# Kernel tuning notes

Hardware: AMD Instinct MI355X
Metric: run time of the kernel (lower is better)

Reference implementation:

```python
import jax, jax.numpy as jnp
import numpy as np

EMBED_DIM = 1024
SHIFT = 0.0

def setup_inputs() -> dict:
    key = jax.random.key(0)
    k1, k2, k3 = jax.random.split(key, 3)
    inputs = jax.random.normal(k1, (4, 2048, EMBED_DIM), dtype=jnp.float32)
    rotation_params = jax.random.normal(k2, (EMBED_DIM, EMBED_DIM), dtype=jnp.float32)
    entangle_params = jax.random.normal(k3, (EMBED_DIM, EMBED_DIM), dtype=jnp.float32)
    return {"inputs": inputs, "rotation_params": rotation_params, "entangle_params": entangle_params}

def reference(inputs, rotation_params, entangle_params):
    # inputs: (b, s, d)
    d = inputs.shape[-1]
    query = jnp.einsum('bsd,de->bse', inputs, rotation_params)
    key = jnp.einsum('bsd,de->bse', inputs, entangle_params)
    scores = jax.nn.softmax(jnp.einsum('bqd,bkd->bqk', query, key) / np.sqrt(d), axis=-1)
    out = jnp.einsum('bqk,bkd->bqd', scores, inputs)
    return jax.nn.sigmoid(out + SHIFT)
```

## Files before the change

kernel.cpp:

```cpp
#include <hip/hip_runtime.h>
#include <hip/hip_bf16.h>
#include <math.h>


using u16 = unsigned short;
using short8 = __attribute__((ext_vector_type(8))) short;
using f32x4  = __attribute__((ext_vector_type(4))) float;

#define MFB(a, b, c) __builtin_amdgcn_mfma_f32_16x16x32_bf16((a), (b), (c), 0, 0, 0)

__device__ static inline u16 f2bf(float f) {
    union { __hip_bfloat16 h; u16 u; } cv; cv.h = __float2bfloat16(f); return cv.u;
}
__device__ static inline float bf2f(u16 u) {
    union { __hip_bfloat16 h; u16 u; } cv; cv.u = u; return __bfloat162float(cv.h);
}
__device__ static inline void split2(float v, u16& h, u16& l) {
    h = f2bf(v);
    l = f2bf(v - bf2f(h));
}

__device__ static inline void gload16(const u16* g, u16* l) {
    __builtin_amdgcn_global_load_lds(
        (const __attribute__((address_space(1))) void*)g,
        (__attribute__((address_space(3))) void*)l, 16, 0, 0);
}

__device__ static inline short8 ldfrag(const u16* sm, int row, int g) {
    const int off = row * 32 + ((g ^ ((row >> 1) & 3)) << 3);
    return *reinterpret_cast<const short8*>(sm + off);
}

enum { EP_F32 = 0, EP_HILO = 1, EP_SIG = 2 };

template<int EPI, bool TRIPLE>
__global__ __launch_bounds__(256)
void gemm_split(const u16* __restrict__ Ahi, const u16* __restrict__ Alo,
                const u16* __restrict__ Bhi, const u16* __restrict__ Blo,
                float* __restrict__ Cf, u16* __restrict__ Chi, u16* __restrict__ Clo,
                int K, int lda, int ldb, int ldc,
                long sA, long sB, long sC, float alpha)
{
    const int z = blockIdx.z;
    Ahi += z * sA;
    Bhi += z * sB;
    if (TRIPLE) { Alo += z * sA; Blo += z * sB; }
    if (EPI == EP_HILO) { Chi += z * sC; Clo += z * sC; }
    else                { Cf  += z * sC; }

    constexpr int BUFSZ  = TRIPLE ? 16384 : 8192;
    constexpr int OFF_BH = TRIPLE ? 8192 : 4096;
    __shared__ __align__(16) u16 smem[2 * BUFSZ];

    const int t = threadIdx.x;
    const int wave = t >> 6, lane = t & 63;
    const int row0 = blockIdx.y * 128, col0 = blockIdx.x * 128;

    const int rr = t >> 2, cc = t & 3;
    const int gg = cc ^ ((rr >> 1) & 3);
    const u16* gAh = Ahi + (long)(row0 + rr) * lda + gg * 8;
    const u16* gBh = Bhi + (long)(col0 + rr) * ldb + gg * 8;
    const u16* gAl = TRIPLE ? (Alo + (long)(row0 + rr) * lda + gg * 8) : nullptr;
    const u16* gBl = TRIPLE ? (Blo + (long)(col0 + rr) * ldb + gg * 8) : nullptr;
    const long a2 = (long)64 * lda, b2 = (long)64 * ldb;

    f32x4 acc[4][4];
    #pragma unroll
    for (int m = 0; m < 4; m++)
        #pragma unroll
        for (int n = 0; n < 4; n++)
            acc[m][n] = (f32x4){0.f, 0.f, 0.f, 0.f};

    const int lr = lane & 15, lg = lane >> 4;
    const int wm = (wave >> 1) * 64, wn = (wave & 1) * 64;
    const int NT = K >> 5;

    {
        u16* d = smem + t * 8;
        gload16(gAh,      d);
        gload16(gAh + a2, d + 2048);
        gload16(gBh,      d + OFF_BH);
        gload16(gBh + b2, d + OFF_BH + 2048);
        if (TRIPLE) {
            gload16(gAl,      d + 4096);
            gload16(gAl + a2, d + 4096 + 2048);
            gload16(gBl,      d + 12288);
            gload16(gBl + b2, d + 12288 + 2048);
        }
    }

    for (int tk = 0; tk < NT; ++tk) {
        __syncthreads();
        const u16* sb = smem + (tk & 1) * BUFSZ;
        if (tk + 1 < NT) {
            const int kn = (tk + 1) << 5;
            u16* d = smem + ((tk + 1) & 1) * BUFSZ + t * 8;
            gload16(gAh + kn,      d);
            gload16(gAh + kn + a2, d + 2048);
            gload16(gBh + kn,      d + OFF_BH);
            gload16(gBh + kn + b2, d + OFF_BH + 2048);
            if (TRIPLE) {
                gload16(gAl + kn,      d + 4096);
                gload16(gAl + kn + a2, d + 4096 + 2048);
                gload16(gBl + kn,      d + 12288);
                gload16(gBl + kn + b2, d + 12288 + 2048);
            }
        }
        const u16* sAh = sb;
        const u16* sAl = sb + 4096;
        const u16* sBh = sb + OFF_BH;
        const u16* sBl = sb + 12288;

        short8 bh[4], bl[4], ah[4], al[4];
        #pragma unroll
        for (int n = 0; n < 4; n++) {
            bh[n] = ldfrag(sBh, wn + n * 16 + lr, lg);
            if (TRIPLE) bl[n] = ldfrag(sBl, wn + n * 16 + lr, lg);
        }
        #pragma unroll
        for (int m = 0; m < 4; m++) {
            ah[m] = ldfrag(sAh, wm + m * 16 + lr, lg);
            if (TRIPLE) al[m] = ldfrag(sAl, wm + m * 16 + lr, lg);
        }
        __builtin_amdgcn_s_setprio(1);
        #pragma unroll
        for (int m = 0; m < 4; m++) {
            #pragma unroll
            for (int n = 0; n < 4; n++) {
                acc[m][n] = MFB(ah[m], bh[n], acc[m][n]);
                if (TRIPLE) {
                    acc[m][n] = MFB(ah[m], bl[n], acc[m][n]);
                    acc[m][n] = MFB(al[m], bh[n], acc[m][n]);
                }
            }
        }
        __builtin_amdgcn_s_setprio(0);
    }

    #pragma unroll
    for (int m = 0; m < 4; m++) {
        #pragma unroll
        for (int n = 0; n < 4; n++) {
            #pragma unroll
            for (int r = 0; r < 4; r++) {
                const int grow = row0 + wm + m * 16 + lg * 4 + r;
                const int gcol = col0 + wn + n * 16 + lr;
                const float v = alpha * acc[m][n][r];
                const long o = (long)grow * ldc + gcol;
                if (EPI == EP_F32) {
                    Cf[o] = v;
                } else if (EPI == EP_SIG) {
                    Cf[o] = 1.0f / (1.0f + __expf(-v));
                } else {
                    u16 h, l; split2(v, h, l);
                    Chi[o] = h; Clo[o] = l;
                }
            }
        }
    }
}

__global__ __launch_bounds__(512)
void gemm_triple_256(const u16* __restrict__ Ahi, const u16* __restrict__ Alo,
                     const u16* __restrict__ Bhi, const u16* __restrict__ Blo,
                     float* __restrict__ Cf,
                     int K, int lda, int ldb, int ldc,
                     long sA, long sB, long sC, float alpha)
{
    const int z = blockIdx.z;
    Ahi += z * sA; Alo += z * sA;
    Bhi += z * sB; Blo += z * sB;
    Cf  += z * sC;

    __shared__ __align__(16) u16 smem[65536];

    const int t = threadIdx.x;
    const int wave = t >> 6, lane = t & 63;
    const int lr = lane & 15, lg = lane >> 4;

    const int u = blockIdx.x + 8 * blockIdx.y;
    const int reg = u & 7, j = u >> 3;
    const int bx = 2 * (reg & 3) + (j & 1);
    const int by = 4 * (reg >> 2) + (j >> 1);
    const int row0 = by * 256, col0 = bx * 256;
    const int wm = (wave >> 2) * 128, wn = (wave & 3) * 64;

    const int srow = t >> 2;
    const int sg = (t & 3) ^ ((srow >> 1) & 3);
    const u16* gAh = Ahi + (long)(row0 + srow) * lda + sg * 8;
    const u16* gAl = Alo + (long)(row0 + srow) * lda + sg * 8;
    const u16* gBh = Bhi + (long)(col0 + srow) * ldb + sg * 8;
    const u16* gBl = Blo + (long)(col0 + srow) * ldb + sg * 8;
    const long a2 = (long)128 * lda, b2 = (long)128 * ldb;

    f32x4 acc[8][4];
    #pragma unroll
    for (int m = 0; m < 8; m++)
        #pragma unroll
        for (int n = 0; n < 4; n++)
            acc[m][n] = (f32x4){0.f, 0.f, 0.f, 0.f};

    const int NT = K >> 5;

    {
        u16* d = smem + t * 8;
        gload16(gAh,      d);          gload16(gAh + a2, d + 4096);
        gload16(gAl,      d + 8192);   gload16(gAl + a2, d + 12288);
        gload16(gBh,      d + 16384);  gload16(gBh + b2, d + 20480);
        gload16(gBl,      d + 24576);  gload16(gBl + b2, d + 28672);
    }

    for (int tk = 0; tk < NT; ++tk) {
        __syncthreads();
        const u16* sb = smem + (tk & 1) * 32768;
        if (tk + 1 < NT) {
            const int kn = (tk + 1) << 5;
            u16* d = smem + ((tk + 1) & 1) * 32768 + t * 8;
            gload16(gAh + kn,      d);          gload16(gAh + kn + a2, d + 4096);
            gload16(gAl + kn,      d + 8192);   gload16(gAl + kn + a2, d + 12288);
            gload16(gBh + kn,      d + 16384);  gload16(gBh + kn + b2, d + 20480);
            gload16(gBl + kn,      d + 24576);  gload16(gBl + kn + b2, d + 28672);
        }
        const u16* sAh = sb;
        const u16* sAl = sb + 8192;
        const u16* sBh = sb + 16384;
        const u16* sBl = sb + 24576;

        short8 bh[4], bl[4], ah[8], al[8];
        #pragma unroll
        for (int n = 0; n < 4; n++) {
            bh[n] = ldfrag(sBh, wn + n * 16 + lr, lg);
            bl[n] = ldfrag(sBl, wn + n * 16 + lr, lg);
        }
        #pragma unroll
        for (int m = 0; m < 8; m++) {
            ah[m] = ldfrag(sAh, wm + m * 16 + lr, lg);
            al[m] = ldfrag(sAl, wm + m * 16 + lr, lg);
        }
        __builtin_amdgcn_s_setprio(1);
        #pragma unroll
        for (int m = 0; m < 8; m++) {
            #pragma unroll
            for (int n = 0; n < 4; n++) {
                acc[m][n] = MFB(ah[m], bh[n], acc[m][n]);
                acc[m][n] = MFB(ah[m], bl[n], acc[m][n]);
                acc[m][n] = MFB(al[m], bh[n], acc[m][n]);
            }
        }
        __builtin_amdgcn_s_setprio(0);
    }

    #pragma unroll
    for (int m = 0; m < 8; m++) {
        #pragma unroll
        for (int n = 0; n < 4; n++) {
            #pragma unroll
            for (int r = 0; r < 4; r++) {
                const int grow = row0 + wm + m * 16 + lg * 4 + r;
                const int gcol = col0 + wn + n * 16 + lr;
                Cf[(long)grow * ldc + gcol] = alpha * acc[m][n][r];
            }
        }
    }
}

__global__ __launch_bounds__(256)
void split_rm3(const float* __restrict__ in0, u16* __restrict__ hi0, u16* __restrict__ lo0, long n0,
               const float* __restrict__ in1, u16* __restrict__ hi1, u16* __restrict__ lo1, long n1,
               const float* __restrict__ in2, u16* __restrict__ hi2, u16* __restrict__ lo2)
{
    long i = ((long)blockIdx.x * 256 + threadIdx.x) * 4;
    const float* in; u16 *hi, *lo;
    if (i < n0)           { in = in0; hi = hi0; lo = lo0; }
    else if (i < n0 + n1) { i -= n0; in = in1; hi = hi1; lo = lo1; }
    else                  { i -= n0 + n1; in = in2; hi = hi2; lo = lo2; }
    const float4 v = *reinterpret_cast<const float4*>(in + i);
    ushort4 h, l;
    split2(v.x, h.x, l.x);
    split2(v.y, h.y, l.y);
    split2(v.z, h.z, l.z);
    split2(v.w, h.w, l.w);
    *reinterpret_cast<ushort4*>(hi + i) = h;
    *reinterpret_cast<ushort4*>(lo + i) = l;
}

__global__ __launch_bounds__(256)
void reduce4_split(const float* __restrict__ p, u16* __restrict__ hi, u16* __restrict__ lo,
                   long n)
{
    const long i = ((long)blockIdx.x * 256 + threadIdx.x) * 4;
    const float4 a = *reinterpret_cast<const float4*>(p + i);
    const float4 b = *reinterpret_cast<const float4*>(p + n + i);
    const float4 c = *reinterpret_cast<const float4*>(p + 2 * n + i);
    const float4 d = *reinterpret_cast<const float4*>(p + 3 * n + i);
    ushort4 h, l;
    split2((a.x + b.x) + (c.x + d.x), h.x, l.x);
    split2((a.y + b.y) + (c.y + d.y), h.y, l.y);
    split2((a.z + b.z) + (c.z + d.z), h.z, l.z);
    split2((a.w + b.w) + (c.w + d.w), h.w, l.w);
    *reinterpret_cast<ushort4*>(hi + i) = h;
    *reinterpret_cast<ushort4*>(lo + i) = l;
}

template<bool HILO>
__global__ __launch_bounds__(256)
void split_tr(const float* __restrict__ in, u16* __restrict__ hi, u16* __restrict__ lo,
              int R, int C, long sIn, long sOut)
{
    in += (long)blockIdx.z * sIn;
    hi += (long)blockIdx.z * sOut;
    if (HILO) lo += (long)blockIdx.z * sOut;

    __shared__ float tile[32][33];
    const int tx = threadIdx.x & 31, ty = threadIdx.x >> 5;
    const int r0 = blockIdx.y * 32, c0 = blockIdx.x * 32;

    #pragma unroll
    for (int j = 0; j < 4; j++)
        tile[ty * 4 + j][tx] = in[(long)(r0 + ty * 4 + j) * C + c0 + tx];
    __syncthreads();

    #pragma unroll
    for (int j = 0; j < 4; j++) {
        const int oc = ty * 4 + j;
        const float v = tile[tx][oc];
        u16 h, l; split2(v, h, l);
        const long o = (long)(c0 + oc) * R + r0 + tx;
        hi[o] = h;
        if (HILO) lo[o] = l;
    }
}

__global__ __launch_bounds__(256)
void softmax_hi(const float* __restrict__ S, u16* __restrict__ hi)
{
    const int NC = 2048;
    const long base = (long)blockIdx.x * NC;
    const float* p = S + base;
    const int tid = threadIdx.x;

    float4 v0 = reinterpret_cast<const float4*>(p)[tid];
    float4 v1 = reinterpret_cast<const float4*>(p)[tid + 256];

    float m = fmaxf(fmaxf(fmaxf(v0.x, v0.y), fmaxf(v0.z, v0.w)),
                    fmaxf(fmaxf(v1.x, v1.y), fmaxf(v1.z, v1.w)));
    #pragma unroll
    for (int off = 1; off < 64; off <<= 1)
        m = fmaxf(m, __shfl_xor(m, off));

    __shared__ float redm[4];
    __shared__ float reds[4];
    const int wave = tid >> 6, lane = tid & 63;
    if (lane == 0) redm[wave] = m;
    __syncthreads();
    m = fmaxf(fmaxf(redm[0], redm[1]), fmaxf(redm[2], redm[3]));

    v0.x = __expf(v0.x - m); v0.y = __expf(v0.y - m);
    v0.z = __expf(v0.z - m); v0.w = __expf(v0.w - m);
    v1.x = __expf(v1.x - m); v1.y = __expf(v1.y - m);
    v1.z = __expf(v1.z - m); v1.w = __expf(v1.w - m);

    float s = (v0.x + v0.y + v0.z + v0.w) + (v1.x + v1.y + v1.z + v1.w);
    #pragma unroll
    for (int off = 1; off < 64; off <<= 1)
        s += __shfl_xor(s, off);
    if (lane == 0) reds[wave] = s;
    __syncthreads();
    s = (reds[0] + reds[1]) + (reds[2] + reds[3]);

    const float inv = 1.0f / s;
    ushort4 h0, h1;
    h0.x = f2bf(v0.x * inv); h0.y = f2bf(v0.y * inv);
    h0.z = f2bf(v0.z * inv); h0.w = f2bf(v0.w * inv);
    h1.x = f2bf(v1.x * inv); h1.y = f2bf(v1.y * inv);
    h1.z = f2bf(v1.z * inv); h1.w = f2bf(v1.w * inv);

    reinterpret_cast<ushort4*>(hi + base)[tid]       = h0;
    reinterpret_cast<ushort4*>(hi + base)[tid + 256] = h1;
}

extern "C" void kernel_launch(void* const* d_in, const int* in_sizes, int n_in,
                              void* d_out, int out_size, void* d_ws, size_t ws_size,
                              hipStream_t stream)
{
    (void)in_sizes; (void)n_in; (void)out_size; (void)ws_size;
    const float* X = (const float*)d_in[0];
    const float* R = (const float*)d_in[1];
    const float* E = (const float*)d_in[2];
    float* out = (float*)d_out;

    const int B = 4, SQ = 2048, D = 1024;
    const long NDX = (long)B * SQ * D;
    const long DD  = (long)D * D;
    const long SS  = (long)B * SQ * SQ;
    const long M16 = 8388608;

    u16* wsu = (u16*)d_ws;
    u16* Xhi  = wsu;
    u16* Xlo  = Xhi + NDX;
    u16* Rhi  = wsu + 2 * M16;
    u16* Rlo  = Rhi + DD;
    u16* Ehi  = Rlo + DD;
    u16* Elo  = Ehi + DD;
    u16* Yhi  = wsu + 2 * M16;
    u16* Ylo  = Yhi + NDX;
    u16* Shi  = wsu + 2 * M16;
    u16* Xthi = wsu;
    float* Wpart = (float*)(wsu + 4 * M16);
    u16* Wthi = wsu + 5 * M16;
    u16* Wtlo = Wthi + DD;
    float* Sf = (float*)(wsu + 4 * M16);

    dim3 thr(256);

    split_rm3<<<dim3((unsigned)((NDX + 2 * DD) / 1024)), thr, 0, stream>>>(
        X, Xhi, Xlo, NDX, R, Rhi, Rlo, DD, E, Ehi, Elo);

    gemm_split<EP_F32, true><<<dim3(D / 128, D / 128, 4), thr, 0, stream>>>(
        Ehi, Elo, Rhi, Rlo, Wpart, nullptr, nullptr,
        256, D, D, D, 256, 256, DD, 1.0f);
    reduce4_split<<<dim3((unsigned)(DD / 1024)), thr, 0, stream>>>(Wpart, Wthi, Wtlo, DD);

    gemm_split<EP_HILO, true><<<dim3(D / 128, (B * SQ) / 128, 1), thr, 0, stream>>>(
        Xhi, Xlo, Wthi, Wtlo, nullptr, Yhi, Ylo,
        D, D, D, D, 0, 0, 0, 1.0f);

    gemm_triple_256<<<dim3(SQ / 256, SQ / 256, B), dim3(512), 0, stream>>>(
        Yhi, Ylo, Xhi, Xlo, Sf,
        D, D, D, SQ,
        (long)SQ * D, (long)SQ * D, (long)SQ * SQ, 0.03125f);

    softmax_hi<<<dim3(B * SQ), thr, 0, stream>>>(Sf, Shi);

    split_tr<false><<<dim3(D / 32, SQ / 32, B), thr, 0, stream>>>(
        X, Xthi, nullptr, SQ, D, (long)SQ * D, (long)SQ * D);

    gemm_split<EP_SIG, false><<<dim3(D / 128, SQ / 128, B), thr, 0, stream>>>(
        Shi, nullptr, Xthi, nullptr, out, nullptr, nullptr,
        SQ, SQ, SQ, D,
        (long)SQ * SQ, (long)SQ * D, (long)SQ * D, 1.0f);
}
```

Baseline: 243.6 us.

## Split GEMM mainloop into four phases with two-tile-ahead staged prefetch

Restructures the split-bf16 GEMM main loop into four sub-phases (quadrants of the 8x4 MFMA tile), interleaving LDS fragment loads with MFMA work. It issues global-to-LDS loads for tile tk+2 into the just-consumed buffer, using explicit vmcnt/lgkmcnt waits and s_barriers instead of one __syncthreads. The aim is to hide both global and LDS latency behind matrix instructions and to reduce register pressure from holding all A fragments at once. It relies on hand-counted waitcnt values and barriers, so there is a risk of races or extra barrier stalls.

```diff
diff --git a/kernel.cpp b/kernel.cpp
--- a/kernel.cpp
+++ b/kernel.cpp
@@ -193,6 +193,21 @@
     const u16* gBl = Blo + (long)(col0 + srow) * ldb + sg * 8;
     const long a2 = (long)128 * lda, b2 = (long)128 * ldb;
 
+    auto STAGE_B = [&](int s, int kk) {
+        u16* d = smem + s * 32768 + t * 8;
+        gload16(gBh + kk,      d + 16384);
+        gload16(gBh + kk + b2, d + 20480);
+        gload16(gBl + kk,      d + 24576);
+        gload16(gBl + kk + b2, d + 28672);
+    };
+    auto STAGE_A = [&](int s, int kk) {
+        u16* d = smem + s * 32768 + t * 8;
+        gload16(gAh + kk,      d);
+        gload16(gAh + kk + a2, d + 4096);
+        gload16(gAl + kk,      d + 8192);
+        gload16(gAl + kk + a2, d + 12288);
+    };
+
     f32x4 acc[8][4];
     #pragma unroll
     for (int m = 0; m < 8; m++)
@@ -202,51 +217,97 @@
 
     const int NT = K >> 5;
 
-    {
-        u16* d = smem + t * 8;
-        gload16(gAh,      d);          gload16(gAh + a2, d + 4096);
-        gload16(gAl,      d + 8192);   gload16(gAl + a2, d + 12288);
-        gload16(gBh,      d + 16384);  gload16(gBh + b2, d + 20480);
-        gload16(gBl,      d + 24576);  gload16(gBl + b2, d + 28672);
-    }
+    STAGE_B(0, 0);  STAGE_A(0, 0);
+    STAGE_B(1, 32); STAGE_A(1, 32);
 
     for (int tk = 0; tk < NT; ++tk) {
-        __syncthreads();
-        const u16* sb = smem + (tk & 1) * 32768;
-        if (tk + 1 < NT) {
-            const int kn = (tk + 1) << 5;
-            u16* d = smem + ((tk + 1) & 1) * 32768 + t * 8;
-            gload16(gAh + kn,      d);          gload16(gAh + kn + a2, d + 4096);
-            gload16(gAl + kn,      d + 8192);   gload16(gAl + kn + a2, d + 12288);
-            gload16(gBh + kn,      d + 16384);  gload16(gBh + kn + b2, d + 20480);
-            gload16(gBl + kn,      d + 24576);  gload16(gBl + kn + b2, d + 28672);
-        }
+        const u16* sb  = smem + (tk & 1) * 32768;
         const u16* sAh = sb;
         const u16* sAl = sb + 8192;
         const u16* sBh = sb + 16384;
         const u16* sBl = sb + 24576;
 
-        short8 bh[4], bl[4], ah[8], al[8];
-        #pragma unroll
-        for (int n = 0; n < 4; n++) {
+        short8 bh[4], bl[4], ah[4], al[4], ah2[4], al2[4];
+
+        if (tk < NT - 1) asm volatile("s_waitcnt vmcnt(8)" ::: "memory");
+        else             asm volatile("s_waitcnt vmcnt(0)" ::: "memory");
+        __builtin_amdgcn_s_barrier();
+        #pragma unroll
+        for (int n = 0; n < 2; n++) {
             bh[n] = ldfrag(sBh, wn + n * 16 + lr, lg);
             bl[n] = ldfrag(sBl, wn + n * 16 + lr, lg);
         }
         #pragma unroll
-        for (int m = 0; m < 8; m++) {
+        for (int m = 0; m < 4; m++) {
             ah[m] = ldfrag(sAh, wm + m * 16 + lr, lg);
             al[m] = ldfrag(sAl, wm + m * 16 + lr, lg);
         }
+        __builtin_amdgcn_s_barrier();
+        asm volatile("s_waitcnt lgkmcnt(0)" ::: "memory");
+        __builtin_amdgcn_sched_barrier(0);
         __builtin_amdgcn_s_setprio(1);
         #pragma unroll
-        for (int m = 0; m < 8; m++) {
-            #pragma unroll
-            for (int n = 0; n < 4; n++) {
+        for (int m = 0; m < 4; m++)
+            #pragma unroll
+            for (int n = 0; n < 2; n++) {
                 acc[m][n] = MFB(ah[m], bh[n], acc[m][n]);
                 acc[m][n] = MFB(ah[m], bl[n], acc[m][n]);
                 acc[m][n] = MFB(al[m], bh[n], acc[m][n]);
             }
-        }
+        __builtin_amdgcn_s_setprio(0);
+
+        __builtin_amdgcn_s_barrier();
+        #pragma unroll
+        for (int n = 2; n < 4; n++) {
+            bh[n] = ldfrag(sBh, wn + n * 16 + lr, lg);
+            bl[n] = ldfrag(sBl, wn + n * 16 + lr, lg);
+        }
+        __builtin_amdgcn_s_barrier();
+        asm volatile("s_waitcnt lgkmcnt(0)" ::: "memory");
+        __builtin_amdgcn_sched_barrier(0);
+        __builtin_amdgcn_s_setprio(1);
+        #pragma unroll
+        for (int m = 0; m < 4; m++)
+            #pragma unroll
+            for (int n = 2; n < 4; n++) {
+                acc[m][n] = MFB(ah[m], bh[n], acc[m][n]);
+                acc[m][n] = MFB(ah[m], bl[n], acc[m][n]);
+                acc[m][n] = MFB(al[m], bh[n], acc[m][n]);
+            }
+        __builtin_amdgcn_s_setprio(0);
+
+        __builtin_amdgcn_s_barrier();
+        #pragma unroll
+        for (int m = 0; m < 4; m++) {
+            ah2[m] = ldfrag(sAh, wm + (4 + m) * 16 + lr, lg);
+            al2[m] = ldfrag(sAl, wm + (4 + m) * 16 + lr, lg);
+        }
+        if (tk + 2 < NT) STAGE_B(tk & 1, (tk + 2) << 5);
+        __builtin_amdgcn_s_barrier();
+        asm volatile("s_waitcnt lgkmcnt(0)" ::: "memory");
+        __builtin_amdgcn_sched_barrier(0);
+        __builtin_amdgcn_s_setprio(1);
+        #pragma unroll
+        for (int m = 0; m < 4; m++)
+            #pragma unroll
+            for (int n = 0; n < 2; n++) {
+                acc[4 + m][n] = MFB(ah2[m], bh[n], acc[4 + m][n]);
+                acc[4 + m][n] = MFB(ah2[m], bl[n], acc[4 + m][n]);
+                acc[4 + m][n] = MFB(al2[m], bh[n], acc[4 + m][n]);
+            }
+        __builtin_amdgcn_s_setprio(0);
+
+        __builtin_amdgcn_s_barrier();
+        if (tk + 2 < NT) STAGE_A(tk & 1, (tk + 2) << 5);
+        __builtin_amdgcn_s_setprio(1);
+        #pragma unroll
+        for (int m = 0; m < 4; m++)
+            #pragma unroll
+            for (int n = 2; n < 4; n++) {
+                acc[4 + m][n] = MFB(ah2[m], bh[n], acc[4 + m][n]);
+                acc[4 + m][n] = MFB(ah2[m], bl[n], acc[4 + m][n]);
+                acc[4 + m][n] = MFB(al2[m], bh[n], acc[4 + m][n]);
+            }
         __builtin_amdgcn_s_setprio(0);
     }
 
```

Result: no change. 244.2 us (+0.3%).

## Use 1024 threads per block in score GEMM with smaller per-wave tiles

Applied to the files above, without the earlier changes.

Raises the score GEMM block from 512 to 1024 threads (16 waves). Each wave now computes a 64x64 subtile instead of 128x64, and each thread issues one load per matrix per stage instead of two. A-fragments are loaded inside the m loop rather than all up front, which cuts accumulator and fragment register pressure. The aim is more waves to hide latency, at the cost of more LDS fragment reads per MFMA, since B fragments are now reused over fewer rows.

```diff
diff --git a/kernel.cpp b/kernel.cpp
--- a/kernel.cpp
+++ b/kernel.cpp
@@ -160,7 +160,7 @@
     }
 }
 
-__global__ __launch_bounds__(512)
+__global__ __launch_bounds__(1024)
 void gemm_triple_256(const u16* __restrict__ Ahi, const u16* __restrict__ Alo,
                      const u16* __restrict__ Bhi, const u16* __restrict__ Blo,
                      float* __restrict__ Cf,
@@ -183,7 +183,7 @@
     const int bx = 2 * (reg & 3) + (j & 1);
     const int by = 4 * (reg >> 2) + (j >> 1);
     const int row0 = by * 256, col0 = bx * 256;
-    const int wm = (wave >> 2) * 128, wn = (wave & 3) * 64;
+    const int wm = (wave >> 2) * 64, wn = (wave & 3) * 64;
 
     const int srow = t >> 2;
     const int sg = (t & 3) ^ ((srow >> 1) & 3);
@@ -191,11 +191,10 @@
     const u16* gAl = Alo + (long)(row0 + srow) * lda + sg * 8;
     const u16* gBh = Bhi + (long)(col0 + srow) * ldb + sg * 8;
     const u16* gBl = Blo + (long)(col0 + srow) * ldb + sg * 8;
-    const long a2 = (long)128 * lda, b2 = (long)128 * ldb;
-
-    f32x4 acc[8][4];
-    #pragma unroll
-    for (int m = 0; m < 8; m++)
+
+    f32x4 acc[4][4];
+    #pragma unroll
+    for (int m = 0; m < 4; m++)
         #pragma unroll
         for (int n = 0; n < 4; n++)
             acc[m][n] = (f32x4){0.f, 0.f, 0.f, 0.f};
@@ -204,10 +203,10 @@
 
     {
         u16* d = smem + t * 8;
-        gload16(gAh,      d);          gload16(gAh + a2, d + 4096);
-        gload16(gAl,      d + 8192);   gload16(gAl + a2, d + 12288);
-        gload16(gBh,      d + 16384);  gload16(gBh + b2, d + 20480);
-        gload16(gBl,      d + 24576);  gload16(gBl + b2, d + 28672);
+        gload16(gAh, d);
+        gload16(gAl, d + 8192);
+        gload16(gBh, d + 16384);
+        gload16(gBl, d + 24576);
     }
 
     for (int tk = 0; tk < NT; ++tk) {
@@ -216,42 +215,39 @@
         if (tk + 1 < NT) {
             const int kn = (tk + 1) << 5;
             u16* d = smem + ((tk + 1) & 1) * 32768 + t * 8;
-            gload16(gAh + kn,      d);          gload16(gAh + kn + a2, d + 4096);
-            gload16(gAl + kn,      d + 8192);   gload16(gAl + kn + a2, d + 12288);
-            gload16(gBh + kn,      d + 16384);  gload16(gBh + kn + b2, d + 20480);
-            gload16(gBl + kn,      d + 24576);  gload16(gBl + kn + b2, d + 28672);
+            gload16(gAh + kn, d);
+            gload16(gAl + kn, d + 8192);
+            gload16(gBh + kn, d + 16384);
+            gload16(gBl + kn, d + 24576);
         }
         const u16* sAh = sb;
         const u16* sAl = sb + 8192;
         const u16* sBh = sb + 16384;
         const u16* sBl = sb + 24576;
 
-        short8 bh[4], bl[4], ah[8], al[8];
+        short8 bh[4], bl[4];
         #pragma unroll
         for (int n = 0; n < 4; n++) {
             bh[n] = ldfrag(sBh, wn + n * 16 + lr, lg);
             bl[n] = ldfrag(sBl, wn + n * 16 + lr, lg);
         }
-        #pragma unroll
-        for (int m = 0; m < 8; m++) {
-            ah[m] = ldfrag(sAh, wm + m * 16 + lr, lg);
-            al[m] = ldfrag(sAl, wm + m * 16 + lr, lg);
-        }
         __builtin_amdgcn_s_setprio(1);
         #pragma unroll
-        for (int m = 0; m < 8; m++) {
+        for (int m = 0; m < 4; m++) {
+            const short8 ah = ldfrag(sAh, wm + m * 16 + lr, lg);
+            const short8 al = ldfrag(sAl, wm + m * 16 + lr, lg);
             #pragma unroll
             for (int n = 0; n < 4; n++) {
-                acc[m][n] = MFB(ah[m], bh[n], acc[m][n]);
-                acc[m][n] = MFB(ah[m], bl[n], acc[m][n]);
-                acc[m][n] = MFB(al[m], bh[n], acc[m][n]);
+                acc[m][n] = MFB(ah, bh[n], acc[m][n]);
+                acc[m][n] = MFB(ah, bl[n], acc[m][n]);
+                acc[m][n] = MFB(al, bh[n], acc[m][n]);
             }
         }
         __builtin_amdgcn_s_setprio(0);
     }
 
     #pragma unroll
-    for (int m = 0; m < 8; m++) {
+    for (int m = 0; m < 4; m++) {
         #pragma unroll
         for (int n = 0; n < 4; n++) {
             #pragma unroll
@@ -425,7 +421,7 @@
         Xhi, Xlo, Wthi, Wtlo, nullptr, Yhi, Ylo,
         D, D, D, D, 0, 0, 0, 1.0f);
 
-    gemm_triple_256<<<dim3(SQ / 256, SQ / 256, B), dim3(512), 0, stream>>>(
+    gemm_triple_256<<<dim3(SQ / 256, SQ / 256, B), dim3(1024), 0, stream>>>(
         Yhi, Ylo, Xhi, Xlo, Sf,
         D, D, D, SQ,
         (long)SQ * D, (long)SQ * D, (long)SQ * SQ, 0.03125f);
```

Result: no change. 242.5 us (-0.4%).
